# Performance work log

Hardware: AMD Instinct MI355X
Metric: run time of the kernel (lower is better)

The kernel has to match this reference:

```python
import jax, jax.numpy as jnp
import numpy as np

N, DIM, H, D, S, B = 30000, 256, 8, 64, 32, 8
INNER = H * D


def setup_inputs() -> dict:
    key = jax.random.key(0)
    ks = jax.random.split(key, 16)
    def w(k, shape, fan_in):
        return jax.random.normal(k, shape, dtype=jnp.float32) / np.sqrt(fan_in)
    x = jax.random.normal(ks[0], (N, DIM), dtype=jnp.float32)
    batch = jnp.sort(jax.random.randint(ks[1], (N,), 0, B))
    return {
        'x': x,
        'batch': batch,
        'W_fx': w(ks[2], (DIM, INNER), DIM), 'b_fx': jnp.zeros((INNER,), jnp.float32),
        'W_x': w(ks[3], (DIM, INNER), DIM), 'b_x': jnp.zeros((INNER,), jnp.float32),
        'W_slice': w(ks[4], (D, S), D), 'b_slice': jnp.zeros((S,), jnp.float32),
        'graph_temp': 0.5 * jnp.ones((1, H, 1), jnp.float32),
        'W_q': w(ks[5], (D, D), D), 'W_k': w(ks[6], (D, D), D), 'W_v': w(ks[7], (D, D), D),
        'W_out': w(ks[8], (INNER, DIM), INNER), 'b_out': jnp.zeros((DIM,), jnp.float32),
    }


def reference(x, batch, W_fx, b_fx, W_x, b_x, W_slice, b_slice, graph_temp,
              W_q, W_k, W_v, W_out, b_out):
    n = x.shape[0]
    scale = D ** -0.5
    fx = (x @ W_fx + b_fx).reshape(n, H, D)   # [N,H,D]
    xm = (x @ W_x + b_x).reshape(n, H, D)     # [N,H,D]
    # per-node slice assignment weights, tempered softmax over slices
    logits = (jnp.einsum('nhd,ds->nhs', xm, W_slice) + b_slice) / graph_temp
    w = jax.nn.softmax(logits, axis=-1)       # [N,H,S]
    onehot = jax.nn.one_hot(batch, B, dtype=x.dtype)  # [N,B]
    # scatter-add pooling per graph: slice_norm[b,h,s], slice_token[b,h,s,d]
    slice_norm = jax.ops.segment_sum(w, batch, num_segments=B)  # [B,H,S]
    wb = w[:, None, :, :] * onehot[:, :, None, None]            # [N,B,H,S]
    slice_token = jnp.einsum('nbhs,nhd->bhsd', wb, fx)
    slice_token = slice_token / (slice_norm[..., None] + 1e-5)
    # small attention over slice tokens
    q = jnp.einsum('bhsd,de->bhse', slice_token, W_q)
    k = jnp.einsum('bhsd,de->bhse', slice_token, W_k)
    v = jnp.einsum('bhsd,de->bhse', slice_token, W_v)
    attn = jax.nn.softmax(jnp.einsum('bhsd,bhtd->bhst', q, k) * scale, axis=-1)
    out_tok = jnp.einsum('bhst,bhtd->bhsd', attn, v)            # [B,H,S,D]
    # gather back to nodes with weighted reduction over slices
    tmp = jnp.einsum('nhs,bhsd->nbhd', w, out_tok)              # [N,B,H,D]
    out_x = jnp.einsum('nb,nbhd->nhd', onehot, tmp).reshape(n, INNER)
    return out_x @ W_out + b_out
```

## Files before the change

### kernel.cpp

```cpp
#include <hip/hip_runtime.h>

#define NDIM 256
#define INNER 512
#define NH 8
#define ND 64
#define NS 32
#define NB 8
#define NP 30208

typedef __attribute__((ext_vector_type(8))) short short8;
typedef __attribute__((ext_vector_type(4))) float f32x4;

static __device__ __forceinline__ short f2bf(float f) {
  unsigned u = __float_as_uint(f);
  unsigned r = (u + 0x7fffu + ((u >> 16) & 1u)) >> 16;
  return (short)r;
}
static __device__ __forceinline__ float bf2f(short s) {
  return __uint_as_float(((unsigned)(unsigned short)s) << 16);
}

static __device__ __forceinline__ void gl_lds16(const void* g, void* l) {
  __builtin_amdgcn_global_load_lds(
      (const __attribute__((address_space(1))) unsigned int*)g,
      (__attribute__((address_space(3))) unsigned int*)l, 16, 0, 0);
}

__global__ __launch_bounds__(256) void k_xsplit(
    const float* __restrict__ x, short* __restrict__ Xh, short* __restrict__ Xl,
    int total4)
{
  int id = blockIdx.x * 256 + threadIdx.x;
  if (id >= total4) return;
  float4 v = *(const float4*)&x[(size_t)id * 4];
  short h0 = f2bf(v.x), h1 = f2bf(v.y), h2 = f2bf(v.z), h3 = f2bf(v.w);
  short4 hv = make_short4(h0, h1, h2, h3);
  short4 lv = make_short4(f2bf(v.x - bf2f(h0)), f2bf(v.y - bf2f(h1)),
                          f2bf(v.z - bf2f(h2)), f2bf(v.w - bf2f(h3)));
  *(short4*)&Xh[(size_t)id * 4] = hv;
  *(short4*)&Xl[(size_t)id * 4] = lv;
}

__global__ __launch_bounds__(256) void k_prep(
    const float* __restrict__ Wfx, const float* __restrict__ Wx,
    const float* __restrict__ bx, const float* __restrict__ Wsl,
    const float* __restrict__ bsl,
    short* __restrict__ Bt1h, short* __restrict__ Bt1l,
    float* __restrict__ bcomb, int* __restrict__ seg)
{
  int id = blockIdx.x * 256 + threadIdx.x;
  if (id < 131072) {
    int k = id >> 9, n = id & 511;
    float v = Wfx[k * 512 + n];
    short hi = f2bf(v); short lo = f2bf(v - bf2f(hi));
    Bt1h[n * 256 + k] = hi; Bt1l[n * 256 + k] = lo;
  } else if (id < 196608) {
    int e = id - 131072;
    int c = e & 255, k = e >> 8;
    int h = c >> 5, s = c & 31;
    float acc = 0.f;
    #pragma unroll 8
    for (int d = 0; d < 64; d++) acc += Wx[k * 512 + h * 64 + d] * Wsl[d * 32 + s];
    short hi = f2bf(acc); short lo = f2bf(acc - bf2f(hi));
    Bt1h[(512 + c) * 256 + k] = hi; Bt1l[(512 + c) * 256 + k] = lo;
  } else if (id < 196864) {
    int c = id - 196608;
    int h = c >> 5, s = c & 31;
    float acc = bsl[s];
    #pragma unroll 8
    for (int d = 0; d < 64; d++) acc += bx[h * 64 + d] * Wsl[d * 32 + s];
    bcomb[c] = acc;
  } else if (id < 196880) {
    int v = id - 196864;
    seg[v] = (v == 0) ? 0 : 0x7fffffff;
  }
}

__global__ __launch_bounds__(256) void k_segs(
    const int* __restrict__ batch, int* __restrict__ seg, int N)
{
  int i = blockIdx.x * 256 + threadIdx.x;
  if (i >= N) return;
  int b = batch[i];
  int p = (i == 0) ? -1 : batch[i - 1];
  for (int v = p + 1; v <= b; v++)
    if (v >= 1) atomicMin(&seg[v], i);
  if (i == N - 1)
    for (int v = b + 1; v <= 8; v++) atomicMin(&seg[v], N);
}

__global__ __launch_bounds__(512, 4) void k_fxw(
    const short* __restrict__ Xh, const short* __restrict__ Xl,
    const short* __restrict__ Bt1h, const short* __restrict__ Bt1l,
    const float* __restrict__ bfx, const float* __restrict__ bcomb,
    const float* __restrict__ gtemp,
    short* __restrict__ fxTh, short* __restrict__ fxTl,
    short* __restrict__ wh_out, short* __restrict__ wl_out,
    int N, int ntiles)
{
  __shared__ __align__(16) short smem[32768];

  const int lid = blockIdx.x;
  const int xcd = lid & 7;
  const int idx = lid >> 3;
  const int ct  = idx % 6;
  const int rowt = xcd + 8 * (idx / 6);
  if (rowt >= ntiles) return;
  const int row0 = rowt * 128;
  const int tid = threadIdx.x;
  const int lane = tid & 63, l15 = lane & 15, quad = lane >> 4;
  const int wvi = tid >> 6;
  const int wm = wvi & 1, wn = wvi >> 1;
  const int ctbase = ct * 128;
  const int srow = lane & 15, schunk = lane >> 4;

  f32x4 acc[4][2];
  #pragma unroll
  for (int i = 0; i < 4; i++)
    #pragma unroll
    for (int j = 0; j < 2; j++) acc[i][j] = (f32x4){0.f, 0.f, 0.f, 0.f};

  int gr = row0 + wvi * 16 + srow;
  if (gr > N - 1) gr = N - 1;
  const int br = ctbase + wvi * 16 + srow;
  const size_t abase = (size_t)gr * 256 + schunk * 8;
  const size_t bbase = (size_t)br * 256 + schunk * 8;

#define STAGE(p, kt_) do {                                         \
    short* base_ = &smem[(p) * 16384];                             \
    gl_lds16(Xh + abase + (kt_) * 32, base_ + wvi * 512);          \
    gl_lds16(Xl + abase + (kt_) * 32, base_ + 4096 + wvi * 512);   \
    gl_lds16(Bt1h + bbase + (kt_) * 32, base_ + 8192 + wvi * 512); \
    gl_lds16(Bt1l + bbase + (kt_) * 32, base_ + 12288 + wvi * 512);\
  } while (0)

  STAGE(0, 0);

  #pragma unroll
  for (int kt = 0; kt < 8; kt++) {
    if (kt < 7) {
      STAGE((kt + 1) & 1, kt + 1);
      asm volatile("s_waitcnt vmcnt(4)" ::: "memory");
    } else {
      asm volatile("s_waitcnt vmcnt(0)" ::: "memory");
    }
    __builtin_amdgcn_s_barrier();
    asm volatile("" ::: "memory");

    const short* AhL = &smem[(kt & 1) * 16384];
    const short* AlL = AhL + 4096;
    const short* BhL = AhL + 8192;
    const short* BlL = AhL + 12288;

    short8 ah[4], al[4];
    #pragma unroll
    for (int mt = 0; mt < 4; mt++) {
      int rg = wm * 4 + mt;
      ah[mt] = *(const short8*)&AhL[rg * 512 + quad * 128 + l15 * 8];
      al[mt] = *(const short8*)&AlL[rg * 512 + quad * 128 + l15 * 8];
    }
    #pragma unroll
    for (int nt = 0; nt < 2; nt++) {
      int rg = wn * 2 + nt;
      short8 bh = *(const short8*)&BhL[rg * 512 + quad * 128 + l15 * 8];
      short8 bl = *(const short8*)&BlL[rg * 512 + quad * 128 + l15 * 8];
      #pragma unroll
      for (int mt = 0; mt < 4; mt++) {
        acc[mt][nt] = __builtin_amdgcn_mfma_f32_16x16x32_bf16(ah[mt], bh, acc[mt][nt], 0, 0, 0);
        acc[mt][nt] = __builtin_amdgcn_mfma_f32_16x16x32_bf16(ah[mt], bl, acc[mt][nt], 0, 0, 0);
        acc[mt][nt] = __builtin_amdgcn_mfma_f32_16x16x32_bf16(al[mt], bh, acc[mt][nt], 0, 0, 0);
      }
    }

    asm volatile("s_waitcnt lgkmcnt(0)" ::: "memory");
    __builtin_amdgcn_s_barrier();
  }
#undef STAGE

  if (ct < 4) {
    short (*T)[136] = (short(*)[136])&smem[0];
    #pragma unroll
    for (int pass = 0; pass < 2; pass++) {
      __syncthreads();
      #pragma unroll
      for (int nt = 0; nt < 2; nt++) {
        int cl = wn * 32 + nt * 16 + l15;
        float bias = bfx[ctbase + cl];
        #pragma unroll
        for (int mt = 0; mt < 4; mt++)
          #pragma unroll
          for (int r = 0; r < 4; r++) {
            int rl = wm * 64 + mt * 16 + quad * 4 + r;
            float v = acc[mt][nt][r] + bias;
            short hi2 = f2bf(v);
            T[cl][rl] = pass ? f2bf(v - bf2f(hi2)) : hi2;
          }
      }
      __syncthreads();
      short* dst = pass ? fxTl : fxTh;
      #pragma unroll
      for (int t = 0; t < 4; t++) {
        int idx2 = tid + t * 512;
        int row = idx2 >> 4, kc = (idx2 & 15) * 8;
        *(int4*)&dst[(size_t)(ctbase + row) * NP + row0 + kc] = *(const int4*)&T[row][kc];
      }
    }
  } else {
    int ct2 = ct - 4;
    int lcbase = ct2 * 128 + wn * 32;
    int h = lcbase >> 5;
    float inv_t = 1.0f / gtemp[h];
    int lc0 = lcbase + l15, lc1 = lcbase + 16 + l15;
    float b0 = bcomb[lc0], b1 = bcomb[lc1];
    #pragma unroll
    for (int mt = 0; mt < 4; mt++) {
      #pragma unroll
      for (int r = 0; r < 4; r++) {
        float s0 = (acc[mt][0][r] + b0) * inv_t;
        float s1 = (acc[mt][1][r] + b1) * inv_t;
        float m = fmaxf(s0, s1);
        #pragma unroll
        for (int off = 1; off < 16; off <<= 1) m = fmaxf(m, __shfl_xor(m, off, 16));
        float e0 = __expf(s0 - m), e1 = __expf(s1 - m);
        float sum = e0 + e1;
        #pragma unroll
        for (int off = 1; off < 16; off <<= 1) sum += __shfl_xor(sum, off, 16);
        float inv = 1.0f / sum;
        int row = row0 + wm * 64 + mt * 16 + quad * 4 + r;
        if (row < N) {
          float w0v = e0 * inv, w1v = e1 * inv;
          size_t base = (size_t)row * (NH * NS);
          short h0 = f2bf(w0v), h1 = f2bf(w1v);
          wh_out[base + lc0] = h0; wl_out[base + lc0] = f2bf(w0v - bf2f(h0));
          wh_out[base + lc1] = h1; wl_out[base + lc1] = f2bf(w1v - bf2f(h1));
        }
      }
    }
  }
}

__global__ __launch_bounds__(256) void k_scat(
    const short* __restrict__ wh, const short* __restrict__ wl,
    const short* __restrict__ fxTh, const short* __restrict__ fxTl,
    const int* __restrict__ seg,
    float* __restrict__ stok, float* __restrict__ snorm, int N)
{
  __shared__ short wth[32][136];
  __shared__ short wtl[32][136];
  __shared__ short fh[64][136];
  __shared__ short fl[64][136];
  __shared__ float ln[32];

  const int h = blockIdx.y;
  const int n0 = blockIdx.x * 512;
  const int tid = threadIdx.x;
  const int lane = tid & 63, l15 = lane & 15, quad = lane >> 4;
  const int wv = tid >> 6;
  const int nend = min(n0 + 512, N);

  f32x4 acc0 = (f32x4){0.f, 0.f, 0.f, 0.f};
  f32x4 acc1 = (f32x4){0.f, 0.f, 0.f, 0.f};

  for (int b = 0; b < NB; b++) {
    int lo = max(seg[b], n0), hi = min(seg[b + 1], nend);
    if (lo >= hi) continue;
    if (tid < 32) ln[tid] = 0.f;
    int c0lo = (lo - n0) & ~127;
    int c0hi = hi - n0;
    for (int c0 = c0lo; c0 < c0hi; c0 += 128) {
      __syncthreads();
      #pragma unroll
      for (int t = 0; t < 2; t++) {
        int idx2 = tid + t * 256;
        int row = idx2 >> 2;
        int sc  = (idx2 & 3) * 8;
        int ng = n0 + c0 + row;
        short8 vh = (short8){0,0,0,0,0,0,0,0};
        short8 vl = (short8){0,0,0,0,0,0,0,0};
        if (ng >= lo && ng < hi) {
          size_t src = (size_t)ng * 256 + h * 32 + sc;
          vh = *(const short8*)&wh[src];
          vl = *(const short8*)&wl[src];
        }
        #pragma unroll
        for (int j = 0; j < 8; j++) {
          wth[sc + j][row] = vh[j];
          wtl[sc + j][row] = vl[j];
        }
      }
      #pragma unroll
      for (int t = 0; t < 4; t++) {
        int idx2 = tid + t * 256;
        int row = idx2 >> 4, kc = (idx2 & 15) * 8;
        size_t src = (size_t)(h * 64 + row) * NP + n0 + c0 + kc;
        *(int4*)&fh[row][kc] = *(const int4*)&fxTh[src];
        *(int4*)&fl[row][kc] = *(const int4*)&fxTl[src];
      }
      __syncthreads();

      {
        int s = tid >> 3, g = tid & 7;
        float sum = 0.f;
        #pragma unroll
        for (int i2 = 0; i2 < 16; i2++) {
          int nl = g * 16 + i2;
          sum += bf2f(wth[s][nl]) + bf2f(wtl[s][nl]);
        }
        atomicAdd(&ln[s], sum);
      }

      for (int k0 = 0; k0 < 128; k0 += 32) {
        int gbase = n0 + c0 + k0;
        if (gbase + 32 <= lo || gbase >= hi) continue;
        short8 a0h = *(const short8*)&wth[l15][k0 + quad * 8];
        short8 a0l = *(const short8*)&wtl[l15][k0 + quad * 8];
        short8 a1h = *(const short8*)&wth[16 + l15][k0 + quad * 8];
        short8 a1l = *(const short8*)&wtl[16 + l15][k0 + quad * 8];
        short8 bh = *(const short8*)&fh[wv * 16 + l15][k0 + quad * 8];
        short8 bl = *(const short8*)&fl[wv * 16 + l15][k0 + quad * 8];
        acc0 = __builtin_amdgcn_mfma_f32_16x16x32_bf16(a0h, bh, acc0, 0, 0, 0);
        acc0 = __builtin_amdgcn_mfma_f32_16x16x32_bf16(a0h, bl, acc0, 0, 0, 0);
        acc0 = __builtin_amdgcn_mfma_f32_16x16x32_bf16(a0l, bh, acc0, 0, 0, 0);
        acc1 = __builtin_amdgcn_mfma_f32_16x16x32_bf16(a1h, bh, acc1, 0, 0, 0);
        acc1 = __builtin_amdgcn_mfma_f32_16x16x32_bf16(a1h, bl, acc1, 0, 0, 0);
        acc1 = __builtin_amdgcn_mfma_f32_16x16x32_bf16(a1l, bh, acc1, 0, 0, 0);
      }
    }
    __syncthreads();
    size_t base = ((size_t)b * NH + h) * NS;
    #pragma unroll
    for (int r = 0; r < 4; r++) {
      atomicAdd(&stok[(base + quad * 4 + r) * ND + wv * 16 + l15], acc0[r]);
      atomicAdd(&stok[(base + 16 + quad * 4 + r) * ND + wv * 16 + l15], acc1[r]);
    }
    if (tid < 32) atomicAdd(&snorm[base + tid], ln[tid]);
    acc0 = (f32x4){0.f, 0.f, 0.f, 0.f};
    acc1 = (f32x4){0.f, 0.f, 0.f, 0.f};
    __syncthreads();
  }
}

__global__ __launch_bounds__(256) void k_attn(
    const float* __restrict__ stok, const float* __restrict__ snorm,
    const float* __restrict__ Wq, const float* __restrict__ Wk,
    const float* __restrict__ Wv, const float* __restrict__ Wout,
    short* __restrict__ PTh, short* __restrict__ PTl)
{
  __shared__ __align__(16) float st[32][68];
  __shared__ __align__(16) float qs[32][68];
  __shared__ __align__(16) float ks[32][68];
  __shared__ __align__(16) float vs[32][68];
  __shared__ __align__(16) float at[32][36];
  __shared__ __align__(16) float ot[32][68];
  __shared__ __align__(16) float wo[64][256];

  const int bh = blockIdx.x;
  const int b = bh >> 3, h = bh & 7;
  const int tid = threadIdx.x;
  const int lane = tid & 63;
  const int wv = tid >> 6;

  {
    const float* wsrc = Wout + (size_t)h * 16384;
    float* wdst = &wo[0][0];
    #pragma unroll
    for (int r = 0; r < 16; r++) {
      int off = r * 1024 + wv * 256;
      gl_lds16(wsrc + off + lane * 4, wdst + off);
    }
  }

  for (int i = tid; i < 2048; i += 256) {
    int ss = i >> 6, dd = i & 63;
    float nrm = snorm[(size_t)bh * NS + ss] + 1e-5f;
    st[ss][dd] = stok[(size_t)bh * 2048 + i] / nrm;
  }
  __syncthreads();

  {
    float aq[8], ak[8], av[8];
    #pragma unroll
    for (int i = 0; i < 8; i++) { aq[i] = 0.f; ak[i] = 0.f; av[i] = 0.f; }
    for (int ch = 0; ch < 16; ch++) {
      float4 sv[8];
      #pragma unroll
      for (int i = 0; i < 8; i++) sv[i] = *(const float4*)&st[wv * 8 + i][ch * 4];
      #pragma unroll
      for (int d = 0; d < 4; d++) {
        int dd = ch * 4 + d;
        float wq = Wq[dd * 64 + lane];
        float wk = Wk[dd * 64 + lane];
        float wvv = Wv[dd * 64 + lane];
        #pragma unroll
        for (int i = 0; i < 8; i++) {
          float sd = (d == 0) ? sv[i].x : (d == 1) ? sv[i].y : (d == 2) ? sv[i].z : sv[i].w;
          aq[i] = fmaf(sd, wq, aq[i]);
          ak[i] = fmaf(sd, wk, ak[i]);
          av[i] = fmaf(sd, wvv, av[i]);
        }
      }
    }
    #pragma unroll
    for (int i = 0; i < 8; i++) {
      qs[wv * 8 + i][lane] = aq[i];
      ks[wv * 8 + i][lane] = ak[i];
      vs[wv * 8 + i][lane] = av[i];
    }
  }
  __syncthreads();

  {
    const int si = tid >> 3, tj0 = (tid & 7) * 4;
    float a0 = 0.f, a1 = 0.f, a2 = 0.f, a3 = 0.f;
    for (int ch = 0; ch < 16; ch++) {
      float4 q4 = *(const float4*)&qs[si][ch * 4];
      float4 k0 = *(const float4*)&ks[tj0 + 0][ch * 4];
      float4 k1 = *(const float4*)&ks[tj0 + 1][ch * 4];
      float4 k2 = *(const float4*)&ks[tj0 + 2][ch * 4];
      float4 k3 = *(const float4*)&ks[tj0 + 3][ch * 4];
      a0 += q4.x * k0.x + q4.y * k0.y + q4.z * k0.z + q4.w * k0.w;
      a1 += q4.x * k1.x + q4.y * k1.y + q4.z * k1.z + q4.w * k1.w;
      a2 += q4.x * k2.x + q4.y * k2.y + q4.z * k2.z + q4.w * k2.w;
      a3 += q4.x * k3.x + q4.y * k3.y + q4.z * k3.z + q4.w * k3.w;
    }
    const float scale = 0.125f;
    *(float4*)&at[si][tj0] = (float4){a0 * scale, a1 * scale, a2 * scale, a3 * scale};
  }
  __syncthreads();

  {
    const int row = tid >> 3, jb = (tid & 7) * 4;
    float4 v = *(const float4*)&at[row][jb];
    float m = fmaxf(fmaxf(v.x, v.y), fmaxf(v.z, v.w));
    #pragma unroll
    for (int off = 1; off < 8; off <<= 1) m = fmaxf(m, __shfl_xor(m, off, 8));
    float e0 = __expf(v.x - m), e1 = __expf(v.y - m);
    float e2 = __expf(v.z - m), e3 = __expf(v.w - m);
    float s = e0 + e1 + e2 + e3;
    #pragma unroll
    for (int off = 1; off < 8; off <<= 1) s += __shfl_xor(s, off, 8);
    float inv = 1.f / s;
    *(float4*)&at[row][jb] = (float4){e0 * inv, e1 * inv, e2 * inv, e3 * inv};
  }
  __syncthreads();

  {
    float acc[8];
    #pragma unroll
    for (int i = 0; i < 8; i++) acc[i] = 0.f;
    for (int ch = 0; ch < 8; ch++) {
      float v0 = vs[ch * 4 + 0][lane];
      float v1 = vs[ch * 4 + 1][lane];
      float v2 = vs[ch * 4 + 2][lane];
      float v3 = vs[ch * 4 + 3][lane];
      #pragma unroll
      for (int i = 0; i < 8; i++) {
        float4 a4 = *(const float4*)&at[wv * 8 + i][ch * 4];
        acc[i] += a4.x * v0 + a4.y * v1 + a4.z * v2 + a4.w * v3;
      }
    }
    #pragma unroll
    for (int i = 0; i < 8; i++) ot[wv * 8 + i][lane] = acc[i];
  }
  __syncthreads();

  {
    const int c0 = 4 * (lane & 31) + 128 * (lane >> 5);
    float pacc[8][4];
    #pragma unroll
    for (int i = 0; i < 8; i++)
      #pragma unroll
      for (int c = 0; c < 4; c++) pacc[i][c] = 0.f;

    for (int ch = 0; ch < 16; ch++) {
      float4 w0 = *(const float4*)&wo[ch * 4 + 0][c0];
      float4 w1 = *(const float4*)&wo[ch * 4 + 1][c0];
      float4 w2 = *(const float4*)&wo[ch * 4 + 2][c0];
      float4 w3 = *(const float4*)&wo[ch * 4 + 3][c0];
      #pragma unroll
      for (int i = 0; i < 8; i++) {
        float4 o4 = *(const float4*)&ot[wv * 8 + i][ch * 4];
        pacc[i][0] = fmaf(o4.x, w0.x, pacc[i][0]);
        pacc[i][1] = fmaf(o4.x, w0.y, pacc[i][1]);
        pacc[i][2] = fmaf(o4.x, w0.z, pacc[i][2]);
        pacc[i][3] = fmaf(o4.x, w0.w, pacc[i][3]);
        pacc[i][0] = fmaf(o4.y, w1.x, pacc[i][0]);
        pacc[i][1] = fmaf(o4.y, w1.y, pacc[i][1]);
        pacc[i][2] = fmaf(o4.y, w1.z, pacc[i][2]);
        pacc[i][3] = fmaf(o4.y, w1.w, pacc[i][3]);
        pacc[i][0] = fmaf(o4.z, w2.x, pacc[i][0]);
        pacc[i][1] = fmaf(o4.z, w2.y, pacc[i][1]);
        pacc[i][2] = fmaf(o4.z, w2.z, pacc[i][2]);
        pacc[i][3] = fmaf(o4.z, w2.w, pacc[i][3]);
        pacc[i][0] = fmaf(o4.w, w3.x, pacc[i][0]);
        pacc[i][1] = fmaf(o4.w, w3.y, pacc[i][1]);
        pacc[i][2] = fmaf(o4.w, w3.z, pacc[i][2]);
        pacc[i][3] = fmaf(o4.w, w3.w, pacc[i][3]);
      }
    }

    #pragma unroll
    for (int cc = 0; cc < 4; cc++) {
      short8 hv, lv;
      #pragma unroll
      for (int i = 0; i < 8; i++) {
        float val = pacc[i][cc];
        short hi = f2bf(val);
        hv[i] = hi;
        lv[i] = f2bf(val - bf2f(hi));
      }
      size_t dst = ((size_t)b * NDIM + (c0 + cc)) * 256 + h * 32 + wv * 8;
      *(short8*)&PTh[dst] = hv;
      *(short8*)&PTl[dst] = lv;
    }
  }
}

__global__ __launch_bounds__(256) void k_outw(
    const short* __restrict__ wh, const short* __restrict__ wl,
    const short* __restrict__ PTh, const short* __restrict__ PTl,
    const int* __restrict__ batch, const float* __restrict__ bout,
    float* __restrict__ out, int N)
{
  __shared__ short Ah[128][40];
  __shared__ short Al[128][40];
  __shared__ short Bh[128][40];
  __shared__ short Bl[128][40];
  __shared__ int b_sh[128];

  const int ct = blockIdx.x;
  const int row0 = blockIdx.y * 128;
  const int tid = threadIdx.x;
  const int lane = tid & 63, l15 = lane & 15, quad = lane >> 4;
  const int wv = tid >> 6, wm = wv & 1, wn = wv >> 1;
  const int ctbase = ct * 128;
  const int cnt = min(128, N - row0);

  if (tid < 128) b_sh[tid] = (tid < cnt) ? batch[row0 + tid] : -1;
  __syncthreads();

  f32x4 acc[4][4];
  #pragma unroll
  for (int i = 0; i < 4; i++)
    #pragma unroll
    for (int j = 0; j < 4; j++) acc[i][j] = (f32x4){0.f, 0.f, 0.f, 0.f};

  int i0 = 0;
  while (i0 < cnt) {
    int b = b_sh[i0];
    int j = i0;
    while (j < cnt && b_sh[j] == b) j++;

    for (int kt = 0; kt < 8; kt++) {
      #pragma unroll
      for (int t = 0; t < 2; t++) {
        int i = tid + t * 256;
        int row = i >> 2, kc = (i & 3) * 8;
        int4 vh = make_int4(0, 0, 0, 0), vl = make_int4(0, 0, 0, 0);
        if (row >= i0 && row < j) {
          size_t src = (size_t)(row0 + row) * 256 + kt * 32 + kc;
          vh = *(const int4*)&wh[src];
          vl = *(const int4*)&wl[src];
        }
        *(int4*)&Ah[row][kc] = vh;
        *(int4*)&Al[row][kc] = vl;
      }
      #pragma unroll
      for (int t = 0; t < 2; t++) {
        int i = tid + t * 256;
        int row = i >> 2, kc = (i & 3) * 8;
        size_t src = ((size_t)b * NDIM + ctbase + row) * 256 + kt * 32 + kc;
        *(int4*)&Bh[row][kc] = *(const int4*)&PTh[src];
        *(int4*)&Bl[row][kc] = *(const int4*)&PTl[src];
      }
      __syncthreads();

      short8 ah[4], al[4];
      #pragma unroll
      for (int mt = 0; mt < 4; mt++) {
        int m = wm * 64 + mt * 16 + l15;
        ah[mt] = *(const short8*)&Ah[m][quad * 8];
        al[mt] = *(const short8*)&Al[m][quad * 8];
      }
      #pragma unroll
      for (int nt = 0; nt < 4; nt++) {
        int n = wn * 64 + nt * 16 + l15;
        short8 bh = *(const short8*)&Bh[n][quad * 8];
        short8 bl = *(const short8*)&Bl[n][quad * 8];
        #pragma unroll
        for (int mt = 0; mt < 4; mt++) {
          acc[mt][nt] = __builtin_amdgcn_mfma_f32_16x16x32_bf16(ah[mt], bh, acc[mt][nt], 0, 0, 0);
          acc[mt][nt] = __builtin_amdgcn_mfma_f32_16x16x32_bf16(ah[mt], bl, acc[mt][nt], 0, 0, 0);
          acc[mt][nt] = __builtin_amdgcn_mfma_f32_16x16x32_bf16(al[mt], bh, acc[mt][nt], 0, 0, 0);
        }
      }
      __syncthreads();
    }
    i0 = j;
  }

  #pragma unroll
  for (int nt = 0; nt < 4; nt++) {
    int c = ctbase + wn * 64 + nt * 16 + l15;
    float bias = bout[c];
    #pragma unroll
    for (int mt = 0; mt < 4; mt++)
      #pragma unroll
      for (int r = 0; r < 4; r++) {
        int row = row0 + wm * 64 + mt * 16 + quad * 4 + r;
        if (row < N) out[(size_t)row * NDIM + c] = acc[mt][nt][r] + bias;
      }
  }
}

extern "C" void kernel_launch(void* const* d_in, const int* in_sizes, int n_in,
                              void* d_out, int out_size, void* d_ws, size_t ws_size,
                              hipStream_t stream) {
  const float* x      = (const float*)d_in[0];
  const int*   batch  = (const int*)d_in[1];
  const float* Wfx    = (const float*)d_in[2];
  const float* bfx    = (const float*)d_in[3];
  const float* Wx     = (const float*)d_in[4];
  const float* bx     = (const float*)d_in[5];
  const float* Wsl    = (const float*)d_in[6];
  const float* bsl    = (const float*)d_in[7];
  const float* gtemp  = (const float*)d_in[8];
  const float* Wq     = (const float*)d_in[9];
  const float* Wk     = (const float*)d_in[10];
  const float* Wv     = (const float*)d_in[11];
  const float* Wout   = (const float*)d_in[12];
  const float* bout   = (const float*)d_in[13];
  float* out = (float*)d_out;

  const int N = in_sizes[0] / NDIM;

  float* stok  = (float*)d_ws;
  float* snorm = stok + 131072;
  float* bcomb = snorm + 2048;
  int*   seg   = (int*)(bcomb + 256);
  short* Bt1h  = (short*)(seg + 16);
  short* Bt1l  = Bt1h + 196608;
  short* Xh    = Bt1l + 196608;
  short* Xl    = Xh + 7680000;
  short* whb   = Xl + 7680000;
  short* wlb   = whb + (size_t)NP * 256;
  short* fxTh  = wlb + (size_t)NP * 256;
  short* fxTl  = fxTh + (size_t)512 * NP;
  short* PTh   = fxTl + (size_t)512 * NP;
  short* PTl   = PTh + 524288;

  hipMemsetAsync(stok, 0, (size_t)(131072 + 2048) * sizeof(float), stream);

  k_xsplit<<<(N * 64 + 255) / 256, 256, 0, stream>>>(x, Xh, Xl, N * 64);

  k_prep<<<770, 256, 0, stream>>>(Wfx, Wx, bx, Wsl, bsl, Bt1h, Bt1l, bcomb, seg);

  k_segs<<<(N + 255) / 256, 256, 0, stream>>>(batch, seg, N);

  const int ntiles = (N + 127) / 128;
  const int qmax = (ntiles + 7) / 8;
  k_fxw<<<8 * qmax * 6, 512, 0, stream>>>(Xh, Xl, Bt1h, Bt1l, bfx, bcomb, gtemp,
                                          fxTh, fxTl, whb, wlb, N, ntiles);

  dim3 g2((N + 511) / 512, NH);
  k_scat<<<g2, 256, 0, stream>>>(whb, wlb, fxTh, fxTl, seg, stok, snorm, N);

  k_attn<<<NB * NH, 256, 0, stream>>>(stok, snorm, Wq, Wk, Wv, Wout, PTh, PTl);

  dim3 g5(2, (N + 127) / 128);
  k_outw<<<g5, 256, 0, stream>>>(whb, wlb, PTh, PTl, batch, bout, out, N);
}
```

Measured before the change: 266.5 us.

## Widen k_fxw column tile from 128 to 256 to halve A-tile reloads

The projection GEMM kernel now computes 256 output columns per block instead of 128, so each wave holds a 4x4 accumulator grid and the grid has half as many blocks. Each block loads two B column chunks per stage and reuses the same X row tile across twice as many columns, cutting the redundant global loads of the hi/lo X split. The epilogues are restructured to write the fx transpose in two halves and to run the slice softmax over two heads per wave. In exchange, LDS use and register pressure rise, occupancy drops (launch bounds lowered to 2) and there are fewer blocks to fill the GPU.

Measured after the change: 279.4 us. 1.05x slower.

```diff
diff --git a/kernel.cpp b/kernel.cpp
--- a/kernel.cpp
+++ b/kernel.cpp
@@ -89,7 +89,7 @@
     for (int v = b + 1; v <= 8; v++) atomicMin(&seg[v], N);
 }
 
-__global__ __launch_bounds__(512, 4) void k_fxw(
+__global__ __launch_bounds__(512, 2) void k_fxw(
     const short* __restrict__ Xh, const short* __restrict__ Xl,
     const short* __restrict__ Bt1h, const short* __restrict__ Bt1l,
     const float* __restrict__ bfx, const float* __restrict__ bcomb,
@@ -98,40 +98,44 @@
     short* __restrict__ wh_out, short* __restrict__ wl_out,
     int N, int ntiles)
 {
-  __shared__ __align__(16) short smem[32768];
+  __shared__ __align__(16) short smem[49152];
 
   const int lid = blockIdx.x;
   const int xcd = lid & 7;
   const int idx = lid >> 3;
-  const int ct  = idx % 6;
-  const int rowt = xcd + 8 * (idx / 6);
+  const int ct2 = idx % 3;
+  const int rowt = xcd + 8 * (idx / 3);
   if (rowt >= ntiles) return;
   const int row0 = rowt * 128;
   const int tid = threadIdx.x;
   const int lane = tid & 63, l15 = lane & 15, quad = lane >> 4;
   const int wvi = tid >> 6;
   const int wm = wvi & 1, wn = wvi >> 1;
-  const int ctbase = ct * 128;
+  const int ctbase = ct2 * 256;
   const int srow = lane & 15, schunk = lane >> 4;
 
-  f32x4 acc[4][2];
+  f32x4 acc[4][4];
   #pragma unroll
   for (int i = 0; i < 4; i++)
     #pragma unroll
-    for (int j = 0; j < 2; j++) acc[i][j] = (f32x4){0.f, 0.f, 0.f, 0.f};
+    for (int j = 0; j < 4; j++) acc[i][j] = (f32x4){0.f, 0.f, 0.f, 0.f};
 
   int gr = row0 + wvi * 16 + srow;
   if (gr > N - 1) gr = N - 1;
-  const int br = ctbase + wvi * 16 + srow;
   const size_t abase = (size_t)gr * 256 + schunk * 8;
-  const size_t bbase = (size_t)br * 256 + schunk * 8;
-
-#define STAGE(p, kt_) do {                                         \
-    short* base_ = &smem[(p) * 16384];                             \
-    gl_lds16(Xh + abase + (kt_) * 32, base_ + wvi * 512);          \
-    gl_lds16(Xl + abase + (kt_) * 32, base_ + 4096 + wvi * 512);   \
-    gl_lds16(Bt1h + bbase + (kt_) * 32, base_ + 8192 + wvi * 512); \
-    gl_lds16(Bt1l + bbase + (kt_) * 32, base_ + 12288 + wvi * 512);\
+  const int bc0 = ctbase + (2 * wvi) * 16 + srow;
+  const int bc1 = ctbase + (2 * wvi + 1) * 16 + srow;
+  const size_t bbase0 = (size_t)bc0 * 256 + schunk * 8;
+  const size_t bbase1 = (size_t)bc1 * 256 + schunk * 8;
+
+#define STAGE(p, kt_) do {                                             \
+    short* base_ = &smem[(p) * 24576];                                 \
+    gl_lds16(Xh + abase + (kt_) * 32, base_ + wvi * 512);              \
+    gl_lds16(Xl + abase + (kt_) * 32, base_ + 4096 + wvi * 512);       \
+    gl_lds16(Bt1h + bbase0 + (kt_) * 32, base_ + 8192 + (2 * wvi) * 512);      \
+    gl_lds16(Bt1h + bbase1 + (kt_) * 32, base_ + 8192 + (2 * wvi + 1) * 512);  \
+    gl_lds16(Bt1l + bbase0 + (kt_) * 32, base_ + 16384 + (2 * wvi) * 512);     \
+    gl_lds16(Bt1l + bbase1 + (kt_) * 32, base_ + 16384 + (2 * wvi + 1) * 512); \
   } while (0)
 
   STAGE(0, 0);
@@ -140,17 +144,17 @@
   for (int kt = 0; kt < 8; kt++) {
     if (kt < 7) {
       STAGE((kt + 1) & 1, kt + 1);
-      asm volatile("s_waitcnt vmcnt(4)" ::: "memory");
+      asm volatile("s_waitcnt vmcnt(6)" ::: "memory");
     } else {
       asm volatile("s_waitcnt vmcnt(0)" ::: "memory");
     }
     __builtin_amdgcn_s_barrier();
     asm volatile("" ::: "memory");
 
-    const short* AhL = &smem[(kt & 1) * 16384];
+    const short* AhL = &smem[(kt & 1) * 24576];
     const short* AlL = AhL + 4096;
     const short* BhL = AhL + 8192;
-    const short* BlL = AhL + 12288;
+    const short* BlL = AhL + 16384;
 
     short8 ah[4], al[4];
     #pragma unroll
@@ -160,8 +164,8 @@
       al[mt] = *(const short8*)&AlL[rg * 512 + quad * 128 + l15 * 8];
     }
     #pragma unroll
-    for (int nt = 0; nt < 2; nt++) {
-      int rg = wn * 2 + nt;
+    for (int nt = 0; nt < 4; nt++) {
+      int rg = wn * 4 + nt;
       short8 bh = *(const short8*)&BhL[rg * 512 + quad * 128 + l15 * 8];
       short8 bl = *(const short8*)&BlL[rg * 512 + quad * 128 + l15 * 8];
       #pragma unroll
@@ -177,62 +181,71 @@
   }
 #undef STAGE
 
-  if (ct < 4) {
+  if (ct2 < 2) {
     short (*T)[136] = (short(*)[136])&smem[0];
     #pragma unroll
-    for (int pass = 0; pass < 2; pass++) {
-      __syncthreads();
-      #pragma unroll
-      for (int nt = 0; nt < 2; nt++) {
-        int cl = wn * 32 + nt * 16 + l15;
-        float bias = bfx[ctbase + cl];
+    for (int h2 = 0; h2 < 2; h2++) {
+      #pragma unroll
+      for (int pass = 0; pass < 2; pass++) {
+        __syncthreads();
+        if ((wn >> 1) == h2) {
+          int cw = wn & 1;
+          #pragma unroll
+          for (int nt = 0; nt < 4; nt++) {
+            int cl = cw * 64 + nt * 16 + l15;
+            float bias = bfx[ctbase + h2 * 128 + cl];
+            #pragma unroll
+            for (int mt = 0; mt < 4; mt++)
+              #pragma unroll
+              for (int r = 0; r < 4; r++) {
+                int rl = wm * 64 + mt * 16 + quad * 4 + r;
+                float v = acc[mt][nt][r] + bias;
+                short hi2 = f2bf(v);
+                T[cl][rl] = pass ? f2bf(v - bf2f(hi2)) : hi2;
+              }
+          }
+        }
+        __syncthreads();
+        short* dst = pass ? fxTl : fxTh;
+        int cb = ctbase + h2 * 128;
         #pragma unroll
-        for (int mt = 0; mt < 4; mt++)
+        for (int t = 0; t < 4; t++) {
+          int idx2 = tid + t * 512;
+          int row = idx2 >> 4, kc = (idx2 & 15) * 8;
+          *(int4*)&dst[(size_t)(cb + row) * NP + row0 + kc] = *(const int4*)&T[row][kc];
+        }
+      }
+    }
+  } else {
+    #pragma unroll
+    for (int hh = 0; hh < 2; hh++) {
+      int lcbase = wn * 64 + hh * 32;
+      int h = lcbase >> 5;
+      float inv_t = 1.0f / gtemp[h];
+      int lc0 = lcbase + l15, lc1 = lcbase + 16 + l15;
+      float b0 = bcomb[lc0], b1 = bcomb[lc1];
+      #pragma unroll
+      for (int mt = 0; mt < 4; mt++) {
+        #pragma unroll
+        for (int r = 0; r < 4; r++) {
+          float s0 = (acc[mt][2 * hh + 0][r] + b0) * inv_t;
+          float s1 = (acc[mt][2 * hh + 1][r] + b1) * inv_t;
+          float m = fmaxf(s0, s1);
           #pragma unroll
-          for (int r = 0; r < 4; r++) {
-            int rl = wm * 64 + mt * 16 + quad * 4 + r;
-            float v = acc[mt][nt][r] + bias;
-            short hi2 = f2bf(v);
-            T[cl][rl] = pass ? f2bf(v - bf2f(hi2)) : hi2;
+          for (int off = 1; off < 16; off <<= 1) m = fmaxf(m, __shfl_xor(m, off, 16));
+          float e0 = __expf(s0 - m), e1 = __expf(s1 - m);
+          float sum = e0 + e1;
+          #pragma unroll
+          for (int off = 1; off < 16; off <<= 1) sum += __shfl_xor(sum, off, 16);
+          float inv = 1.0f / sum;
+          int row = row0 + wm * 64 + mt * 16 + quad * 4 + r;
+          if (row < N) {
+            float w0v = e0 * inv, w1v = e1 * inv;
+            size_t base = (size_t)row * (NH * NS);
+            short h0 = f2bf(w0v), h1 = f2bf(w1v);
+            wh_out[base + lc0] = h0; wl_out[base + lc0] = f2bf(w0v - bf2f(h0));
+            wh_out[base + lc1] = h1; wl_out[base + lc1] = f2bf(w1v - bf2f(h1));
           }
-      }
-      __syncthreads();
-      short* dst = pass ? fxTl : fxTh;
-      #pragma unroll
-      for (int t = 0; t < 4; t++) {
-        int idx2 = tid + t * 512;
-        int row = idx2 >> 4, kc = (idx2 & 15) * 8;
-        *(int4*)&dst[(size_t)(ctbase + row) * NP + row0 + kc] = *(const int4*)&T[row][kc];
-      }
-    }
-  } else {
-    int ct2 = ct - 4;
-    int lcbase = ct2 * 128 + wn * 32;
-    int h = lcbase >> 5;
-    float inv_t = 1.0f / gtemp[h];
-    int lc0 = lcbase + l15, lc1 = lcbase + 16 + l15;
-    float b0 = bcomb[lc0], b1 = bcomb[lc1];
-    #pragma unroll
-    for (int mt = 0; mt < 4; mt++) {
-      #pragma unroll
-      for (int r = 0; r < 4; r++) {
-        float s0 = (acc[mt][0][r] + b0) * inv_t;
-        float s1 = (acc[mt][1][r] + b1) * inv_t;
-        float m = fmaxf(s0, s1);
-        #pragma unroll
-        for (int off = 1; off < 16; off <<= 1) m = fmaxf(m, __shfl_xor(m, off, 16));
-        float e0 = __expf(s0 - m), e1 = __expf(s1 - m);
-        float sum = e0 + e1;
-        #pragma unroll
-        for (int off = 1; off < 16; off <<= 1) sum += __shfl_xor(sum, off, 16);
-        float inv = 1.0f / sum;
-        int row = row0 + wm * 64 + mt * 16 + quad * 4 + r;
-        if (row < N) {
-          float w0v = e0 * inv, w1v = e1 * inv;
-          size_t base = (size_t)row * (NH * NS);
-          short h0 = f2bf(w0v), h1 = f2bf(w1v);
-          wh_out[base + lc0] = h0; wl_out[base + lc0] = f2bf(w0v - bf2f(h0));
-          wh_out[base + lc1] = h1; wl_out[base + lc1] = f2bf(w1v - bf2f(h1));
         }
       }
     }
@@ -659,7 +672,7 @@
 
   const int ntiles = (N + 127) / 128;
   const int qmax = (ntiles + 7) / 8;
-  k_fxw<<<8 * qmax * 6, 512, 0, stream>>>(Xh, Xl, Bt1h, Bt1l, bfx, bcomb, gtemp,
+  k_fxw<<<8 * qmax * 3, 512, 0, stream>>>(Xh, Xl, Bt1h, Bt1l, bfx, bcomb, gtemp,
                                           fxTh, fxTl, whb, wlb, N, ntiles);
 
   dim3 g2((N + 511) / 512, NH);
```

## Use direct-to-LDS loads with swizzle and double buffering in scatter and output kernels

Applied to the files above, without the earlier changes.

In the scatter kernel, the fx tile is now loaded with global_load_lds straight into an unpadded, XOR-swizzled shared buffer, and the MFMA operand reads are swizzled to match. In the output kernel, row tiles that all belong to one graph take a new fast path: double-buffered global-to-LDS staging with explicit vmcnt waits and raw barriers, so the next k-slice loads while MFMAs run on the current one. Mixed-graph tiles keep the original path. The intent is to hide global load latency and cut LDS bank conflicts and register staging, at the cost of more complex synchronisation and a larger shared-memory footprint.

Result: no change. 268.9 us (+0.9%).

```diff
diff --git a/kernel.cpp b/kernel.cpp
--- a/kernel.cpp
+++ b/kernel.cpp
@@ -247,8 +247,8 @@
 {
   __shared__ short wth[32][136];
   __shared__ short wtl[32][136];
-  __shared__ short fh[64][136];
-  __shared__ short fl[64][136];
+  __shared__ __align__(16) short fh[64][128];
+  __shared__ __align__(16) short fl[64][128];
   __shared__ float ln[32];
 
   const int h = blockIdx.y;
@@ -257,6 +257,7 @@
   const int lane = tid & 63, l15 = lane & 15, quad = lane >> 4;
   const int wv = tid >> 6;
   const int nend = min(n0 + 512, N);
+  const int lr4 = lane >> 4, lc16 = lane & 15;
 
   f32x4 acc0 = (f32x4){0.f, 0.f, 0.f, 0.f};
   f32x4 acc1 = (f32x4){0.f, 0.f, 0.f, 0.f};
@@ -269,6 +270,17 @@
     int c0hi = hi - n0;
     for (int c0 = c0lo; c0 < c0hi; c0 += 128) {
       __syncthreads();
+
+      #pragma unroll
+      for (int t = 0; t < 4; t++) {
+        int i = wv * 4 + t;
+        int row = i * 4 + lr4;
+        int cs = lc16 ^ (row & 7);
+        size_t src = (size_t)(h * 64 + row) * NP + n0 + c0 + cs * 8;
+        gl_lds16(fxTh + src, &fh[i * 4][0]);
+        gl_lds16(fxTl + src, &fl[i * 4][0]);
+      }
+
       #pragma unroll
       for (int t = 0; t < 2; t++) {
         int idx2 = tid + t * 256;
@@ -288,14 +300,6 @@
           wtl[sc + j][row] = vl[j];
         }
       }
-      #pragma unroll
-      for (int t = 0; t < 4; t++) {
-        int idx2 = tid + t * 256;
-        int row = idx2 >> 4, kc = (idx2 & 15) * 8;
-        size_t src = (size_t)(h * 64 + row) * NP + n0 + c0 + kc;
-        *(int4*)&fh[row][kc] = *(const int4*)&fxTh[src];
-        *(int4*)&fl[row][kc] = *(const int4*)&fxTl[src];
-      }
       __syncthreads();
 
       {
@@ -316,8 +320,10 @@
         short8 a0l = *(const short8*)&wtl[l15][k0 + quad * 8];
         short8 a1h = *(const short8*)&wth[16 + l15][k0 + quad * 8];
         short8 a1l = *(const short8*)&wtl[16 + l15][k0 + quad * 8];
-        short8 bh = *(const short8*)&fh[wv * 16 + l15][k0 + quad * 8];
-        short8 bl = *(const short8*)&fl[wv * 16 + l15][k0 + quad * 8];
+        int rB = wv * 16 + l15;
+        int cB = ((k0 >> 3) + quad) ^ (rB & 7);
+        short8 bh = *(const short8*)&fh[rB][cB * 8];
+        short8 bl = *(const short8*)&fl[rB][cB * 8];
         acc0 = __builtin_amdgcn_mfma_f32_16x16x32_bf16(a0h, bh, acc0, 0, 0, 0);
         acc0 = __builtin_amdgcn_mfma_f32_16x16x32_bf16(a0h, bl, acc0, 0, 0, 0);
         acc0 = __builtin_amdgcn_mfma_f32_16x16x32_bf16(a0l, bh, acc0, 0, 0, 0);
@@ -522,10 +528,7 @@
     const int* __restrict__ batch, const float* __restrict__ bout,
     float* __restrict__ out, int N)
 {
-  __shared__ short Ah[128][40];
-  __shared__ short Al[128][40];
-  __shared__ short Bh[128][40];
-  __shared__ short Bl[128][40];
+  __shared__ __align__(16) short smem[32768];
   __shared__ int b_sh[128];
 
   const int ct = blockIdx.x;
@@ -545,48 +548,59 @@
     #pragma unroll
     for (int j = 0; j < 4; j++) acc[i][j] = (f32x4){0.f, 0.f, 0.f, 0.f};
 
-  int i0 = 0;
-  while (i0 < cnt) {
-    int b = b_sh[i0];
-    int j = i0;
-    while (j < cnt && b_sh[j] == b) j++;
-
+  const bool uniform = (cnt == 128) && (b_sh[0] == b_sh[127]);
+
+  if (uniform) {
+    const int b = b_sh[0];
+    const int lr = lane >> 2;
+    const int csw = (lane & 3) ^ ((lane >> 3) & 3);
+    const size_t aoff = (size_t)(row0 + wv * 32 + lr) * 256 + csw * 8;
+    const size_t boff = ((size_t)b * 256 + ctbase + wv * 32 + lr) * 256 + csw * 8;
+
+#define OSTAGE(p, kt_) do {                                                    \
+    short* base_ = &smem[(p) * 16384];                                         \
+    gl_lds16(wh + aoff + (kt_) * 32,        base_ + (wv * 32) * 32);           \
+    gl_lds16(wh + aoff + (kt_) * 32 + 4096, base_ + (wv * 32 + 16) * 32);      \
+    gl_lds16(wl + aoff + (kt_) * 32,        base_ + 4096 + (wv * 32) * 32);    \
+    gl_lds16(wl + aoff + (kt_) * 32 + 4096, base_ + 4096 + (wv * 32 + 16) * 32);\
+    gl_lds16(PTh + boff + (kt_) * 32,        base_ + 8192 + (wv * 32) * 32);   \
+    gl_lds16(PTh + boff + (kt_) * 32 + 4096, base_ + 8192 + (wv * 32 + 16) * 32);\
+    gl_lds16(PTl + boff + (kt_) * 32,        base_ + 12288 + (wv * 32) * 32);  \
+    gl_lds16(PTl + boff + (kt_) * 32 + 4096, base_ + 12288 + (wv * 32 + 16) * 32);\
+  } while (0)
+
+    OSTAGE(0, 0);
+
+    #pragma unroll
     for (int kt = 0; kt < 8; kt++) {
-      #pragma unroll
-      for (int t = 0; t < 2; t++) {
-        int i = tid + t * 256;
-        int row = i >> 2, kc = (i & 3) * 8;
-        int4 vh = make_int4(0, 0, 0, 0), vl = make_int4(0, 0, 0, 0);
-        if (row >= i0 && row < j) {
-          size_t src = (size_t)(row0 + row) * 256 + kt * 32 + kc;
-          vh = *(const int4*)&wh[src];
-          vl = *(const int4*)&wl[src];
-        }
-        *(int4*)&Ah[row][kc] = vh;
-        *(int4*)&Al[row][kc] = vl;
-      }
-      #pragma unroll
-      for (int t = 0; t < 2; t++) {
-        int i = tid + t * 256;
-        int row = i >> 2, kc = (i & 3) * 8;
-        size_t src = ((size_t)b * NDIM + ctbase + row) * 256 + kt * 32 + kc;
-        *(int4*)&Bh[row][kc] = *(const int4*)&PTh[src];
-        *(int4*)&Bl[row][kc] = *(const int4*)&PTl[src];
-      }
-      __syncthreads();
+      if (kt < 7) {
+        OSTAGE((kt + 1) & 1, kt + 1);
+        asm volatile("s_waitcnt vmcnt(8)" ::: "memory");
+      } else {
+        asm volatile("s_waitcnt vmcnt(0)" ::: "memory");
+      }
+      __builtin_amdgcn_s_barrier();
+      asm volatile("" ::: "memory");
+
+      const short* AhL = &smem[(kt & 1) * 16384];
+      const short* AlL = AhL + 4096;
+      const short* BhL = AhL + 8192;
+      const short* BlL = AhL + 12288;
 
       short8 ah[4], al[4];
       #pragma unroll
       for (int mt = 0; mt < 4; mt++) {
         int m = wm * 64 + mt * 16 + l15;
-        ah[mt] = *(const short8*)&Ah[m][quad * 8];
-        al[mt] = *(const short8*)&Al[m][quad * 8];
+        int q2 = quad ^ ((m >> 1) & 3);
+        ah[mt] = *(const short8*)&AhL[m * 32 + q2 * 8];
+        al[mt] = *(const short8*)&AlL[m * 32 + q2 * 8];
       }
       #pragma unroll
       for (int nt = 0; nt < 4; nt++) {
         int n = wn * 64 + nt * 16 + l15;
-        short8 bh = *(const short8*)&Bh[n][quad * 8];
-        short8 bl = *(const short8*)&Bl[n][quad * 8];
+        int q2 = quad ^ ((n >> 1) & 3);
+        short8 bh = *(const short8*)&BhL[n * 32 + q2 * 8];
+        short8 bl = *(const short8*)&BlL[n * 32 + q2 * 8];
         #pragma unroll
         for (int mt = 0; mt < 4; mt++) {
           acc[mt][nt] = __builtin_amdgcn_mfma_f32_16x16x32_bf16(ah[mt], bh, acc[mt][nt], 0, 0, 0);
@@ -594,9 +608,70 @@
           acc[mt][nt] = __builtin_amdgcn_mfma_f32_16x16x32_bf16(al[mt], bh, acc[mt][nt], 0, 0, 0);
         }
       }
-      __syncthreads();
-    }
-    i0 = j;
+
+      asm volatile("s_waitcnt lgkmcnt(0)" ::: "memory");
+      __builtin_amdgcn_s_barrier();
+    }
+#undef OSTAGE
+  } else {
+    short (*Ah)[40] = (short(*)[40])&smem[0];
+    short (*Al)[40] = (short(*)[40])&smem[5120];
+    short (*Bh)[40] = (short(*)[40])&smem[10240];
+    short (*Bl)[40] = (short(*)[40])&smem[15360];
+
+    int i0 = 0;
+    while (i0 < cnt) {
+      int b = b_sh[i0];
+      int j = i0;
+      while (j < cnt && b_sh[j] == b) j++;
+
+      for (int kt = 0; kt < 8; kt++) {
+        #pragma unroll
+        for (int t = 0; t < 2; t++) {
+          int i = tid + t * 256;
+          int row = i >> 2, kc = (i & 3) * 8;
+          int4 vh = make_int4(0, 0, 0, 0), vl = make_int4(0, 0, 0, 0);
+          if (row >= i0 && row < j) {
+            size_t src = (size_t)(row0 + row) * 256 + kt * 32 + kc;
+            vh = *(const int4*)&wh[src];
+            vl = *(const int4*)&wl[src];
+          }
+          *(int4*)&Ah[row][kc] = vh;
+          *(int4*)&Al[row][kc] = vl;
+        }
+        #pragma unroll
+        for (int t = 0; t < 2; t++) {
+          int i = tid + t * 256;
+          int row = i >> 2, kc = (i & 3) * 8;
+          size_t src = ((size_t)b * NDIM + ctbase + row) * 256 + kt * 32 + kc;
+          *(int4*)&Bh[row][kc] = *(const int4*)&PTh[src];
+          *(int4*)&Bl[row][kc] = *(const int4*)&PTl[src];
+        }
+        __syncthreads();
+
+        short8 ah[4], al[4];
+        #pragma unroll
+        for (int mt = 0; mt < 4; mt++) {
+          int m = wm * 64 + mt * 16 + l15;
+          ah[mt] = *(const short8*)&Ah[m][quad * 8];
+          al[mt] = *(const short8*)&Al[m][quad * 8];
+        }
+        #pragma unroll
+        for (int nt = 0; nt < 4; nt++) {
+          int n = wn * 64 + nt * 16 + l15;
+          short8 bh = *(const short8*)&Bh[n][quad * 8];
+          short8 bl = *(const short8*)&Bl[n][quad * 8];
+          #pragma unroll
+          for (int mt = 0; mt < 4; mt++) {
+            acc[mt][nt] = __builtin_amdgcn_mfma_f32_16x16x32_bf16(ah[mt], bh, acc[mt][nt], 0, 0, 0);
+            acc[mt][nt] = __builtin_amdgcn_mfma_f32_16x16x32_bf16(ah[mt], bl, acc[mt][nt], 0, 0, 0);
+            acc[mt][nt] = __builtin_amdgcn_mfma_f32_16x16x32_bf16(al[mt], bh, acc[mt][nt], 0, 0, 0);
+          }
+        }
+        __syncthreads();
+      }
+      i0 = j;
+    }
   }
 
   #pragma unroll
```
